# Performance work log

Measured on AMD Instinct MI355X. Metric: run time of the kernel, lower is better.

Reference implementation:

```python
import jax, jax.numpy as jnp
import numpy as np

EPS = 1e-5

@jax.custom_vjp
def binarize(x):
    return jnp.sign(x)

def _bin_fwd(x):
    return jnp.sign(x), None

def _bin_bwd(_, g):
    return (g,)  # straight-through estimator (matches .data overwrite trick)

binarize.defvjp(_bin_fwd, _bin_bwd)

def conv2d(x, w, b):
    y = jax.lax.conv_general_dilated(x, w, (1, 1), 'VALID',
                                     dimension_numbers=('NCHW', 'OIHW', 'NCHW'))
    return y + b[None, :, None, None]

def bn2d(x, g, be, m, v):
    inv = g / jnp.sqrt(v + EPS)
    return (x - m[None, :, None, None]) * inv[None, :, None, None] + be[None, :, None, None]

def bn1d(x, m, v):  # affine=False, eval mode
    return (x - m) / jnp.sqrt(v + EPS)

def maxpool2(x):
    return jax.lax.reduce_window(x, -jnp.inf, jax.lax.max, (1, 1, 2, 2), (1, 1, 2, 2), 'VALID')

def hardtanh(x):
    return jnp.clip(x, -1.0, 1.0)

def setup_inputs() -> dict:
    key = jax.random.key(0)
    ks = jax.random.split(key, 16)
    B = 8192
    d = {
        'x': jax.random.normal(ks[0], (B, 3, 32, 32), jnp.float32),
        'w1': jax.random.normal(ks[1], (16, 3, 5, 5), jnp.float32),
        'b1': jax.random.normal(ks[2], (16,), jnp.float32) * 0.1,
        'g1': jnp.ones((16,), jnp.float32), 'be1': jnp.zeros((16,), jnp.float32),
        'm1': jnp.zeros((16,), jnp.float32), 'v1': jnp.ones((16,), jnp.float32),
        'w2': jax.random.normal(ks[3], (32, 16, 5, 5), jnp.float32),
        'b2': jax.random.normal(ks[4], (32,), jnp.float32) * 0.1,
        'g2': jnp.ones((32,), jnp.float32), 'be2': jnp.zeros((32,), jnp.float32),
        'm2': jnp.zeros((32,), jnp.float32), 'v2': jnp.ones((32,), jnp.float32),
        'w3': jax.random.normal(ks[5], (64, 32, 5, 5), jnp.float32),
        'b3': jax.random.normal(ks[6], (64,), jnp.float32) * 0.1,
        'g3': jnp.ones((64,), jnp.float32), 'be3': jnp.zeros((64,), jnp.float32),
        'm3': jnp.zeros((64,), jnp.float32), 'v3': jnp.ones((64,), jnp.float32),
        'fw1': jax.random.normal(ks[7], (128, 64), jnp.float32),
        'fb1': jax.random.normal(ks[8], (128,), jnp.float32) * 0.1,
        'cm1': jnp.zeros((128,), jnp.float32), 'cv1': jnp.ones((128,), jnp.float32),
        'fw2': jax.random.normal(ks[9], (128, 128), jnp.float32),
        'fb2': jax.random.normal(ks[10], (128,), jnp.float32) * 0.1,
        'cm2': jnp.zeros((128,), jnp.float32), 'cv2': jnp.ones((128,), jnp.float32),
        'fw3': jax.random.normal(ks[11], (10, 128), jnp.float32),
        'cm3': jnp.zeros((10,), jnp.float32), 'cv3': jnp.ones((10,), jnp.float32),
    }
    return d

def reference(x, w1, b1, g1, be1, m1, v1, w2, b2, g2, be2, m2, v2,
              w3, b3, g3, be3, m3, v3, fw1, fb1, cm1, cv1,
              fw2, fb2, cm2, cv2, fw3, cm3, cv3):
    # features: conv1 input has 3 channels -> NOT binarized (first-layer rule)
    h = conv2d(x, binarize(w1), b1)
    h = maxpool2(hardtanh(bn2d(h, g1, be1, m1, v1)))
    h = conv2d(binarize(h), binarize(w2), b2)
    h = maxpool2(hardtanh(bn2d(h, g2, be2, m2, v2)))
    h = conv2d(binarize(h), binarize(w3), b3)
    h = hardtanh(bn2d(h, g3, be3, m3, v3))
    h = h.reshape(-1, 64)  # spatial is 1x1 by construction
    # classifier (all linear inputs binarized: in_features != 784)
    h = binarize(h) @ binarize(fw1).T + fb1
    h = bn1d(h, cm1, cv1)
    h = binarize(h) @ binarize(fw2).T + fb2
    h = bn1d(h, cm2, cv2)
    h = binarize(h) @ binarize(fw3).T
    h = bn1d(h, cm3, cv3)
    return jax.nn.log_softmax(h, axis=-1)
```

## Files before the change

### kernel.cpp

```cpp
#include <hip/hip_runtime.h>
#include <cstdint>

#define EPS 1e-5f

#define A1_OFF   0ull
#define W2M_OFF  4030464ull
#define W3M_OFF  4033664ull
#define FW1M_OFF 4040064ull
#define FW2M_OFF 4041088ull
#define FW3M_OFF 4043136ull
#define T1_OFF   4043296ull
#define T2_OFF   4043360ull
#define T3_OFF   4043488ull
#define TC1_OFF  4043744ull
#define TC2_OFF  4044256ull
#define BF_OFF   4044768ull
#define FIXCNT_OFF 4061184ull
#define FIXREC_OFF 4061248ull
#define FIXCAP   32768u

using bf16x8 = __attribute__((ext_vector_type(8))) short;
using f32x4  = __attribute__((ext_vector_type(4))) float;

union FragU { unsigned int u[4]; bf16x8 f; };

__device__ inline unsigned short rne_bf16(float f) {
    unsigned int u = __float_as_uint(f);
    return (unsigned short)((u + 0x7FFFu + ((u >> 16) & 1u)) >> 16);
}

__global__ void setup_kernel(
    const float* __restrict__ w1, const float* __restrict__ w2,
    const float* __restrict__ w3,
    const float* __restrict__ fw1, const float* __restrict__ fw2,
    const float* __restrict__ fw3,
    const float* __restrict__ b1, const float* __restrict__ g1,
    const float* __restrict__ be1, const float* __restrict__ m1,
    const float* __restrict__ v1,
    const float* __restrict__ b2, const float* __restrict__ g2,
    const float* __restrict__ be2, const float* __restrict__ m2,
    const float* __restrict__ v2,
    const float* __restrict__ b3, const float* __restrict__ g3,
    const float* __restrict__ be3, const float* __restrict__ m3,
    const float* __restrict__ v3,
    const float* __restrict__ fb1, const float* __restrict__ cm1,
    const float* __restrict__ fb2, const float* __restrict__ cm2,
    unsigned int* __restrict__ w2m, unsigned int* __restrict__ w3m,
    unsigned long long* __restrict__ fw1m, unsigned long long* __restrict__ fw2m,
    unsigned long long* __restrict__ fw3m,
    float* __restrict__ t1, float* __restrict__ t2, float* __restrict__ t3,
    float* __restrict__ tc1, float* __restrict__ tc2,
    uint4* __restrict__ bfrag, unsigned int* __restrict__ fixcnt)
{
    const int tid = threadIdx.x;
    const int blk = blockIdx.x;

    if (blk == 0) {
        if (tid < 16) t1[tid] = m1[tid] - be1[tid]*sqrtf(v1[tid]+EPS)/g1[tid] - b1[tid];
        if (tid < 32) t2[tid] = m2[tid] - be2[tid]*sqrtf(v2[tid]+EPS)/g2[tid] - b2[tid];
        if (tid < 64) t3[tid] = m3[tid] - be3[tid]*sqrtf(v3[tid]+EPS)/g3[tid] - b3[tid];
        if (tid < 128) { tc1[tid] = cm1[tid] - fb1[tid]; tc2[tid] = cm2[tid] - fb2[tid]; }
        for (int t = tid; t < 32*25; t += 256) {
            int oc = t / 25, pos = t % 25;
            unsigned int mk = 0;
            for (int ic = 0; ic < 16; ++ic)
                if (w2[(oc*16 + ic)*25 + pos] > 0.0f) mk |= 1u << ic;
            w2m[t] = mk;
        }
    } else if (blk == 1) {
        for (int t = tid; t < 64*25; t += 256) {
            int oc = t / 25, pos = t % 25;
            unsigned int mk = 0;
            for (int ic = 0; ic < 32; ++ic)
                if (w3[(oc*32 + ic)*25 + pos] > 0.0f) mk |= 1u << ic;
            w3m[t] = mk;
        }
    } else if (blk == 2) {
        for (int t = tid; t < 128; t += 256) {
            unsigned long long mk = 0;
            for (int i = 0; i < 64; ++i)
                if (fw1[t*64 + i] > 0.0f) mk |= 1ull << i;
            fw1m[t] = mk;
        }
    } else if (blk == 3) {
        for (int t = tid; t < 128; t += 256) {
            unsigned long long lo = 0, hi = 0;
            for (int i = 0; i < 64; ++i) {
                if (fw2[t*128 + i]      > 0.0f) lo |= 1ull << i;
                if (fw2[t*128 + 64 + i] > 0.0f) hi |= 1ull << i;
            }
            fw2m[2*t] = lo; fw2m[2*t+1] = hi;
        }
        if (tid < 10) {
            unsigned long long lo = 0, hi = 0;
            for (int i = 0; i < 64; ++i) {
                if (fw3[tid*128 + i]      > 0.0f) lo |= 1ull << i;
                if (fw3[tid*128 + 64 + i] > 0.0f) hi |= 1ull << i;
            }
            fw3m[2*tid] = lo; fw3m[2*tid+1] = hi;
        }
    } else {
        if (tid == 0) fixcnt[0] = 0;
        if (tid < 64) {
            const int oc = tid & 15, q = tid >> 4;
            for (int d = 0; d < 4; ++d)
                for (int kg = 0; kg < 4; ++kg) {
                    int ck = kg*4 + q;
                    unsigned short s[8];
                    for (int j = 0; j < 8; ++j) {
                        int kx = j - d;
                        unsigned short v = 0;
                        if (ck < 15 && kx >= 0 && kx < 5)
                            v = (w1[oc*75 + ck*5 + kx] > 0.0f) ? 0x3F80 : 0xBF80;
                        s[j] = v;
                    }
                    uint4 o;
                    o.x = (unsigned int)s[0] | ((unsigned int)s[1] << 16);
                    o.y = (unsigned int)s[2] | ((unsigned int)s[3] << 16);
                    o.z = (unsigned int)s[4] | ((unsigned int)s[5] << 16);
                    o.w = (unsigned int)s[6] | ((unsigned int)s[7] << 16);
                    bfrag[(d*4 + kg)*64 + tid] = o;
                }
        }
    }
}

__global__ __launch_bounds__(256, 3) void convpool1_kernel(
    const float* __restrict__ x, const float* __restrict__ t1,
    const uint4* __restrict__ bfrag, unsigned int* __restrict__ a1u,
    unsigned int* __restrict__ fixcnt, uint2* __restrict__ fixrec)
{
    __shared__ alignas(16) unsigned short xh[3*36*44];
    __shared__ alignas(16) unsigned short xl[3*36*44];
    __shared__ unsigned short pk16[196];

    const int tid  = threadIdx.x;
    const int lane = tid & 63;
    const int wv   = tid >> 6;
    const int quad = lane >> 4;
    const int me   = lane & 15;
    const int n0   = blockIdx.x * 8;

    FragU B[16];
    #pragma unroll
    for (int i = 0; i < 16; ++i)
        *(uint4*)B[i].u = bfrag[i*64 + lane];

    const float thr = t1[me];
    #pragma unroll 1
    for (int i = -1; i < 8; ++i) {
        float4 st[3];
        const int more = (i < 7);
        if (more) {
            const float4* xg = (const float4*)(x + (size_t)(n0 + i + 1) * 3072);
            #pragma unroll
            for (int k = 0; k < 3; ++k) st[k] = xg[tid + k*256];
        }

        if (i >= 0) {
            const int n = n0 + i;
            #pragma unroll 1
            for (int ti = 0; ti < 4; ++ti) {
                const int task = wv + ti*4;
                if (task >= 14) break;
                const int g = task >> 1, tt = task & 1;

                f32x4 acc[4];
                #pragma unroll
                for (int d = 0; d < 4; ++d) acc[d] = (f32x4){0.f, 0.f, 0.f, 0.f};

                #pragma unroll
                for (int kg = 0; kg < 4; ++kg) {
                    int ck = kg*4 + quad;
                    int ckc = ck < 15 ? ck : 14;
                    int c = ckc / 5, ky = ckc % 5;
                    int idx = (c*36 + ky + me + tt*16)*44 + 4*g;
                    FragU ah, al;
                    uint2 p0 = *(const uint2*)&xh[idx];
                    uint2 p1 = *(const uint2*)&xh[idx + 4];
                    ah.u[0] = p0.x; ah.u[1] = p0.y; ah.u[2] = p1.x; ah.u[3] = p1.y;
                    uint2 q0 = *(const uint2*)&xl[idx];
                    uint2 q1 = *(const uint2*)&xl[idx + 4];
                    al.u[0] = q0.x; al.u[1] = q0.y; al.u[2] = q1.x; al.u[3] = q1.y;
                    #pragma unroll
                    for (int d = 0; d < 4; ++d)
                        acc[d] = __builtin_amdgcn_mfma_f32_16x16x32_bf16(
                            ah.f, B[d*4 + kg].f, acc[d], 0, 0, 0);
                    #pragma unroll
                    for (int d = 0; d < 4; ++d)
                        acc[d] = __builtin_amdgcn_mfma_f32_16x16x32_bf16(
                            al.f, B[d*4 + kg].f, acc[d], 0, 0, 0);
                }

                const int valid = !(tt == 1 && quad == 3);
                #pragma unroll
                for (int dp = 0; dp < 2; ++dp) {
                    f32x4 A0 = acc[2*dp], A1 = acc[2*dp + 1];
                    #pragma unroll
                    for (int r = 0; r < 2; ++r) {
                        float h = fmaxf(fmaxf(A0[2*r], A0[2*r+1]),
                                        fmaxf(A1[2*r], A1[2*r+1]));
                        int bit = h > thr;
                        if (valid && fabsf(h - thr) < 2e-3f) {
                            int cell = (tt*8 + quad*2 + r)*14 + 2*g + dp;
                            unsigned int slot = atomicAdd(fixcnt, 1u);
                            if (slot < FIXCAP) {
                                uint2 rec;
                                rec.x = (unsigned int)n;
                                rec.y = ((unsigned int)cell << 8) | (unsigned int)me;
                                fixrec[slot] = rec;
                            }
                        }
                        unsigned long long mk = __ballot(bit);
                        if (me == 0 && valid)
                            pk16[(tt*8 + quad*2 + r)*14 + 2*g + dp] =
                                (unsigned short)(mk >> (quad*16));
                    }
                }
            }
        }
        __syncthreads();

        if (i >= 0 && tid < 98)
            a1u[(size_t)(n0 + i)*98 + tid] =
                (unsigned int)pk16[2*tid] | ((unsigned int)pk16[2*tid + 1] << 16);
        if (more) {
            #pragma unroll
            for (int k = 0; k < 3; ++k) {
                float4 v = st[k];
                int j = tid + k*256;
                int c = j >> 8, f = j & 255, row = f >> 3, q = f & 7;
                int e = (c*36 + row)*44 + 4*q;
                unsigned short h0 = rne_bf16(v.x), h1 = rne_bf16(v.y),
                               h2 = rne_bf16(v.z), h3 = rne_bf16(v.w);
                float r0 = v.x - __uint_as_float((unsigned int)h0 << 16);
                float r1 = v.y - __uint_as_float((unsigned int)h1 << 16);
                float r2 = v.z - __uint_as_float((unsigned int)h2 << 16);
                float r3 = v.w - __uint_as_float((unsigned int)h3 << 16);
                uint2 ph, pl;
                ph.x = (unsigned int)h0 | ((unsigned int)h1 << 16);
                ph.y = (unsigned int)h2 | ((unsigned int)h3 << 16);
                pl.x = (unsigned int)rne_bf16(r0) | ((unsigned int)rne_bf16(r1) << 16);
                pl.y = (unsigned int)rne_bf16(r2) | ((unsigned int)rne_bf16(r3) << 16);
                *(uint2*)&xh[e] = ph;
                *(uint2*)&xl[e] = pl;
            }
        }
        __syncthreads();
    }
}

__global__ void fixup_kernel(
    const float* __restrict__ x, const float* __restrict__ w1,
    const float* __restrict__ t1,
    const unsigned int* __restrict__ fixcnt, const uint2* __restrict__ fixrec,
    unsigned int* __restrict__ a1u)
{
    unsigned int cnt = fixcnt[0];
    if (cnt > FIXCAP) cnt = FIXCAP;
    for (unsigned int i = blockIdx.x*blockDim.x + threadIdx.x; i < cnt;
         i += gridDim.x*blockDim.x) {
        uint2 rec = fixrec[i];
        int n = (int)rec.x;
        int cell = (int)(rec.y >> 8);
        int oc = (int)(rec.y & 255u);
        int py = cell / 14, px = cell % 14;
        float thr = t1[oc];
        double best = -1e300;
        #pragma unroll 1
        for (int d2 = 0; d2 < 4; ++d2) {
            int oy = 2*py + (d2 >> 1), ox = 2*px + (d2 & 1);
            double s = 0.0;
            #pragma unroll 1
            for (int c2 = 0; c2 < 3; ++c2)
                #pragma unroll 1
                for (int ky2 = 0; ky2 < 5; ++ky2)
                    #pragma unroll 1
                    for (int kx2 = 0; kx2 < 5; ++kx2) {
                        float wv = w1[oc*75 + c2*25 + ky2*5 + kx2];
                        float xv = x[(size_t)n*3072 + c2*1024 + (oy + ky2)*32 + ox + kx2];
                        s += (wv > 0.0f) ? (double)xv : -(double)xv;
                    }
            best = fmax(best, s);
        }
        unsigned int mask = 1u << ((cell & 1)*16 + oc);
        unsigned int* wp = &a1u[(size_t)n*98 + (cell >> 1)];
        if (best > (double)thr) atomicOr(wp, mask);
        else                    atomicAnd(wp, ~mask);
    }
}

__global__ __launch_bounds__(256) void conv2tail_kernel(
    const unsigned int* __restrict__ a1u, const unsigned int* __restrict__ w2m,
    const float* __restrict__ t2,
    const unsigned int* __restrict__ w3m, const float* __restrict__ t3,
    const unsigned long long* __restrict__ fw1m, const float* __restrict__ tc1,
    const unsigned long long* __restrict__ fw2m, const float* __restrict__ tc2,
    const unsigned long long* __restrict__ fw3m,
    const float* __restrict__ cm3, const float* __restrict__ cv3,
    float* __restrict__ out)
{
    __shared__ unsigned int M[8][14][16];
    __shared__ unsigned int P[8][14][16];
    __shared__ unsigned int Q[8][13][16];
    __shared__ unsigned int a2l[8][25];
    __shared__ unsigned int w3s[1600];
    __shared__ unsigned long long fw1s[128], fw2s[256], fw3s[20];
    __shared__ float t3s[64], tc1s[128], tc2s[128], cm3s[16], cv3s[16];

    const int tid = threadIdx.x;
    const int lane = tid & 63;
    const int wv = tid >> 6;
    const int n0 = blockIdx.x * 8;

    for (int i = tid; i < 1600; i += 256) w3s[i] = w3m[i];
    if (tid < 128) { fw1s[tid] = fw1m[tid]; tc1s[tid] = tc1[tid]; tc2s[tid] = tc2[tid]; }
    fw2s[tid] = fw2m[tid];
    if (tid < 20) fw3s[tid] = fw3m[tid];
    if (tid < 64) t3s[tid] = t3[tid];
    if (tid < 10) { cm3s[tid] = cm3[tid]; cv3s[tid] = cv3[tid]; }

    for (int i = tid; i < 8*98; i += 256) {
        unsigned int v = a1u[(size_t)n0*98 + i];
        int e = 2*i;
        int im = e / 196, r = e - im*196;
        int y0 = r / 14, c0 = r - y0*14;
        int r1 = r + 1, y1 = r1 / 14, c1 = r1 - y1*14;
        M[im][y0][c0] = v & 0xffffu;
        M[im][y1][c1] = v >> 16;
    }
    __syncthreads();
    for (int i = tid; i < 8*14*13; i += 256) {
        int im = i / 182, r = i - im*182, y = r / 13, j = r - y*13;
        P[im][y][j] = M[im][y][j] | (M[im][y][j+1] << 16);
    }
    for (int i = tid; i < 8*13*14; i += 256) {
        int im = i / 182, r = i - im*182, y = r / 14, j = r - y*14;
        Q[im][y][j] = M[im][y][j] | (M[im][y+1][j] << 16);
    }
    __syncthreads();

    const int img = tid >> 5, oc = tid & 31;
    unsigned int wrow[25];
    #pragma unroll
    for (int k = 0; k < 25; ++k) wrow[k] = w2m[oc*25 + k];
    unsigned int wp[5][2], wc0, wc1, wcs;
    #pragma unroll
    for (int ky = 0; ky < 5; ++ky) {
        wp[ky][0] = wrow[ky*5]     | (wrow[ky*5+1] << 16);
        wp[ky][1] = wrow[ky*5 + 2] | (wrow[ky*5+3] << 16);
    }
    wc0 = wrow[4]  | (wrow[9]  << 16);
    wc1 = wrow[14] | (wrow[19] << 16);
    wcs = wrow[24];
    const float thr = t2[oc];

    unsigned int bits = 0;
    int hprev[5];
    #pragma unroll 2
    for (int oy = 0; oy < 10; ++oy) {
        unsigned int Pr[5][12];
        #pragma unroll
        for (int ky = 0; ky < 5; ++ky) {
            const uint4* pr = (const uint4*)&P[img][oy + ky][0];
            uint4 a = pr[0], b = pr[1], c = pr[2];
            Pr[ky][0]=a.x; Pr[ky][1]=a.y; Pr[ky][2]=a.z; Pr[ky][3]=a.w;
            Pr[ky][4]=b.x; Pr[ky][5]=b.y; Pr[ky][6]=b.z; Pr[ky][7]=b.w;
            Pr[ky][8]=c.x; Pr[ky][9]=c.y; Pr[ky][10]=c.z; Pr[ky][11]=c.w;
        }
        unsigned int Qa[10], Qb[10], Ms[10];
        {
            const uint4* qa = (const uint4*)&Q[img][oy][4];
            const uint2* qa2 = (const uint2*)&Q[img][oy][12];
            uint4 a = qa[0], b = qa[1]; uint2 c = qa2[0];
            Qa[0]=a.x; Qa[1]=a.y; Qa[2]=a.z; Qa[3]=a.w;
            Qa[4]=b.x; Qa[5]=b.y; Qa[6]=b.z; Qa[7]=b.w; Qa[8]=c.x; Qa[9]=c.y;
            const uint4* qb = (const uint4*)&Q[img][oy+2][4];
            const uint2* qb2 = (const uint2*)&Q[img][oy+2][12];
            uint4 d = qb[0], e = qb[1]; uint2 f = qb2[0];
            Qb[0]=d.x; Qb[1]=d.y; Qb[2]=d.z; Qb[3]=d.w;
            Qb[4]=e.x; Qb[5]=e.y; Qb[6]=e.z; Qb[7]=e.w; Qb[8]=f.x; Qb[9]=f.y;
            const uint4* ms = (const uint4*)&M[img][oy+4][4];
            const uint2* ms2 = (const uint2*)&M[img][oy+4][12];
            uint4 g = ms[0], h = ms[1]; uint2 k2 = ms2[0];
            Ms[0]=g.x; Ms[1]=g.y; Ms[2]=g.z; Ms[3]=g.w;
            Ms[4]=h.x; Ms[5]=h.y; Ms[6]=h.z; Ms[7]=h.w; Ms[8]=k2.x; Ms[9]=k2.y;
        }
        int X[10];
        #pragma unroll
        for (int ox = 0; ox < 10; ++ox) {
            int s = 0;
            #pragma unroll
            for (int ky = 0; ky < 5; ++ky)
                s += __popc(Pr[ky][ox] ^ wp[ky][0]) + __popc(Pr[ky][ox+2] ^ wp[ky][1]);
            s += __popc(Qa[ox] ^ wc0) + __popc(Qb[ox] ^ wc1) + __popc(Ms[ox] ^ wcs);
            X[ox] = s;
        }
        #pragma unroll
        for (int px = 0; px < 5; ++px) {
            int h = min(X[2*px], X[2*px+1]);
            if ((oy & 1) == 0) hprev[px] = h;
            else {
                int mn = min(hprev[px], h);
                if ((float)(400 - 2*mn) > thr) bits |= 1u << ((oy >> 1)*5 + px);
            }
        }
    }
    #pragma unroll
    for (int cell = 0; cell < 25; ++cell) {
        unsigned long long m = __ballot((bits >> cell) & 1);
        if (lane == 0)  a2l[2*wv][cell]     = (unsigned int)m;
        if (lane == 32) a2l[2*wv + 1][cell] = (unsigned int)(m >> 32);
    }
    __syncthreads();

    #pragma unroll 1
    for (int rnd = 0; rnd < 2; ++rnd) {
        const int im = wv + 4*rnd;
        const int n = n0 + im;

        unsigned int av[25];
        #pragma unroll
        for (int k = 0; k < 25; ++k) av[k] = a2l[im][k];

        int X = 0;
        #pragma unroll
        for (int k = 0; k < 25; ++k) X += __popc(av[k] ^ w3s[lane*25 + k]);
        float d3 = (float)(800 - 2*X);
        unsigned long long a3 = __ballot(d3 > t3s[lane]);

        int o1 = lane + 64;
        int d0 = 64 - 2*(int)__popcll(a3 ^ fw1s[lane]);
        int d1 = 64 - 2*(int)__popcll(a3 ^ fw1s[o1]);
        unsigned long long a4lo = __ballot((float)d0 > tc1s[lane]);
        unsigned long long a4hi = __ballot((float)d1 > tc1s[o1]);

        int e0 = 128 - 2*(int)(__popcll(a4lo ^ fw2s[2*lane]) + __popcll(a4hi ^ fw2s[2*lane+1]));
        int e1 = 128 - 2*(int)(__popcll(a4lo ^ fw2s[2*o1])   + __popcll(a4hi ^ fw2s[2*o1+1]));
        unsigned long long a5lo = __ballot((float)e0 > tc2s[lane]);
        unsigned long long a5hi = __ballot((float)e1 > tc2s[o1]);

        float y = -1e30f;
        if (lane < 10) {
            int f = 128 - 2*(int)(__popcll(a5lo ^ fw3s[2*lane]) + __popcll(a5hi ^ fw3s[2*lane+1]));
            y = ((float)f - cm3s[lane]) / sqrtf(cv3s[lane] + EPS);
        }
        float mx = y;
        #pragma unroll
        for (int off = 8; off > 0; off >>= 1) mx = fmaxf(mx, __shfl_xor(mx, off, 16));
        float s = (lane < 10) ? expf(y - mx) : 0.0f;
        #pragma unroll
        for (int off = 8; off > 0; off >>= 1) s += __shfl_xor(s, off, 16);
        if (lane < 10) out[(size_t)n*10 + lane] = y - mx - logf(s);
    }
}

extern "C" void kernel_launch(void* const* d_in, const int* in_sizes, int n_in,
                              void* d_out, int out_size, void* d_ws, size_t ws_size,
                              hipStream_t stream)
{
    const float* x   = (const float*)d_in[0];
    const float* w1  = (const float*)d_in[1];
    const float* b1  = (const float*)d_in[2];
    const float* g1  = (const float*)d_in[3];
    const float* be1 = (const float*)d_in[4];
    const float* m1  = (const float*)d_in[5];
    const float* v1  = (const float*)d_in[6];
    const float* w2  = (const float*)d_in[7];
    const float* b2  = (const float*)d_in[8];
    const float* g2  = (const float*)d_in[9];
    const float* be2 = (const float*)d_in[10];
    const float* m2  = (const float*)d_in[11];
    const float* v2  = (const float*)d_in[12];
    const float* w3  = (const float*)d_in[13];
    const float* b3  = (const float*)d_in[14];
    const float* g3  = (const float*)d_in[15];
    const float* be3 = (const float*)d_in[16];
    const float* m3  = (const float*)d_in[17];
    const float* v3  = (const float*)d_in[18];
    const float* fw1 = (const float*)d_in[19];
    const float* fb1 = (const float*)d_in[20];
    const float* cm1 = (const float*)d_in[21];
    const float* fw2 = (const float*)d_in[23];
    const float* fb2 = (const float*)d_in[24];
    const float* cm2 = (const float*)d_in[25];
    const float* fw3 = (const float*)d_in[27];
    const float* cm3 = (const float*)d_in[28];
    const float* cv3 = (const float*)d_in[29];

    char* ws = (char*)d_ws;
    unsigned int*       a1u  = (unsigned int*)(ws + A1_OFF);
    unsigned int*       w2m  = (unsigned int*)(ws + W2M_OFF);
    unsigned int*       w3m  = (unsigned int*)(ws + W3M_OFF);
    unsigned long long* fw1m = (unsigned long long*)(ws + FW1M_OFF);
    unsigned long long* fw2m = (unsigned long long*)(ws + FW2M_OFF);
    unsigned long long* fw3m = (unsigned long long*)(ws + FW3M_OFF);
    float* t1  = (float*)(ws + T1_OFF);
    float* t2  = (float*)(ws + T2_OFF);
    float* t3  = (float*)(ws + T3_OFF);
    float* tc1 = (float*)(ws + TC1_OFF);
    float* tc2 = (float*)(ws + TC2_OFF);
    uint4* bfrag = (uint4*)(ws + BF_OFF);
    unsigned int* fixcnt = (unsigned int*)(ws + FIXCNT_OFF);
    uint2* fixrec = (uint2*)(ws + FIXREC_OFF);

    setup_kernel<<<5, 256, 0, stream>>>(
        w1, w2, w3, fw1, fw2, fw3,
        b1, g1, be1, m1, v1,
        b2, g2, be2, m2, v2,
        b3, g3, be3, m3, v3,
        fb1, cm1, fb2, cm2,
        w2m, w3m, fw1m, fw2m, fw3m, t1, t2, t3, tc1, tc2, bfrag, fixcnt);

    convpool1_kernel<<<1024, 256, 0, stream>>>(x, t1, bfrag, a1u, fixcnt, fixrec);
    fixup_kernel<<<64, 256, 0, stream>>>(x, w1, t1, fixcnt, fixrec, a1u);
    conv2tail_kernel<<<1024, 256, 0, stream>>>(a1u, w2m, t2, w3m, t3,
                                               fw1m, tc1, fw2m, tc2, fw3m,
                                               cm3, cv3, (float*)d_out);
}
```

Before: 342.6 us.

## Shrink conv1 blocks to two waves, drop register prefetch, balance tasks per wave

The conv1+pool kernel now runs 128-thread blocks over 4 images each on a grid of 2048 blocks instead of 256 threads over 8 images. The register-staged prefetch of the next image is removed: each iteration loads and converts its own image, then syncs and computes. With two waves, each wave now handles exactly 7 of the 14 tasks, which removes the uneven 4/4/3/3 split. LDS base offsets are precomputed outside the loop. The aim is better wave balance, lower register pressure and more resident blocks, at the cost of losing the overlap between global loads and MFMA work inside a block.

```diff
diff --git a/kernel.cpp b/kernel.cpp
--- a/kernel.cpp
+++ b/kernel.cpp
@@ -125,7 +125,7 @@
     }
 }
 
-__global__ __launch_bounds__(256, 3) void convpool1_kernel(
+__global__ __launch_bounds__(128) void convpool1_kernel(
     const float* __restrict__ x, const float* __restrict__ t1,
     const uint4* __restrict__ bfrag, unsigned int* __restrict__ a1u,
     unsigned int* __restrict__ fixcnt, uint2* __restrict__ fixrec)
@@ -139,115 +139,121 @@
     const int wv   = tid >> 6;
     const int quad = lane >> 4;
     const int me   = lane & 15;
-    const int n0   = blockIdx.x * 8;
+    const int n0   = blockIdx.x * 4;
 
     FragU B[16];
     #pragma unroll
     for (int i = 0; i < 16; ++i)
         *(uint4*)B[i].u = bfrag[i*64 + lane];
 
+    int basekg[4];
+    #pragma unroll
+    for (int kg = 0; kg < 4; ++kg) {
+        int ck = kg*4 + quad;
+        int ckc = ck < 15 ? ck : 14;
+        int c = ckc / 5, ky = ckc % 5;
+        basekg[kg] = (c*36 + ky + me)*44;
+    }
+    int se[6];
+    #pragma unroll
+    for (int k = 0; k < 6; ++k) {
+        int j = tid + k*128;
+        int c = j >> 8, f = j & 255, row = f >> 3, q = f & 7;
+        se[k] = (c*36 + row)*44 + 4*q;
+    }
+
     const float thr = t1[me];
     #pragma unroll 1
-    for (int i = -1; i < 8; ++i) {
-        float4 st[3];
-        const int more = (i < 7);
-        if (more) {
-            const float4* xg = (const float4*)(x + (size_t)(n0 + i + 1) * 3072);
+    for (int i = 0; i < 4; ++i) {
+        if (i > 0 && tid < 98)
+            a1u[(size_t)(n0 + i - 1)*98 + tid] =
+                (unsigned int)pk16[2*tid] | ((unsigned int)pk16[2*tid + 1] << 16);
+        {
+            const float4* xg = (const float4*)(x + (size_t)(n0 + i) * 3072);
+            float4 v[6];
             #pragma unroll
-            for (int k = 0; k < 3; ++k) st[k] = xg[tid + k*256];
-        }
-
-        if (i >= 0) {
-            const int n = n0 + i;
-            #pragma unroll 1
-            for (int ti = 0; ti < 4; ++ti) {
-                const int task = wv + ti*4;
-                if (task >= 14) break;
-                const int g = task >> 1, tt = task & 1;
-
-                f32x4 acc[4];
-                #pragma unroll
-                for (int d = 0; d < 4; ++d) acc[d] = (f32x4){0.f, 0.f, 0.f, 0.f};
-
-                #pragma unroll
-                for (int kg = 0; kg < 4; ++kg) {
-                    int ck = kg*4 + quad;
-                    int ckc = ck < 15 ? ck : 14;
-                    int c = ckc / 5, ky = ckc % 5;
-                    int idx = (c*36 + ky + me + tt*16)*44 + 4*g;
-                    FragU ah, al;
-                    uint2 p0 = *(const uint2*)&xh[idx];
-                    uint2 p1 = *(const uint2*)&xh[idx + 4];
-                    ah.u[0] = p0.x; ah.u[1] = p0.y; ah.u[2] = p1.x; ah.u[3] = p1.y;
-                    uint2 q0 = *(const uint2*)&xl[idx];
-                    uint2 q1 = *(const uint2*)&xl[idx + 4];
-                    al.u[0] = q0.x; al.u[1] = q0.y; al.u[2] = q1.x; al.u[3] = q1.y;
-                    #pragma unroll
-                    for (int d = 0; d < 4; ++d)
-                        acc[d] = __builtin_amdgcn_mfma_f32_16x16x32_bf16(
-                            ah.f, B[d*4 + kg].f, acc[d], 0, 0, 0);
-                    #pragma unroll
-                    for (int d = 0; d < 4; ++d)
-                        acc[d] = __builtin_amdgcn_mfma_f32_16x16x32_bf16(
-                            al.f, B[d*4 + kg].f, acc[d], 0, 0, 0);
-                }
-
-                const int valid = !(tt == 1 && quad == 3);
-                #pragma unroll
-                for (int dp = 0; dp < 2; ++dp) {
-                    f32x4 A0 = acc[2*dp], A1 = acc[2*dp + 1];
-                    #pragma unroll
-                    for (int r = 0; r < 2; ++r) {
-                        float h = fmaxf(fmaxf(A0[2*r], A0[2*r+1]),
-                                        fmaxf(A1[2*r], A1[2*r+1]));
-                        int bit = h > thr;
-                        if (valid && fabsf(h - thr) < 2e-3f) {
-                            int cell = (tt*8 + quad*2 + r)*14 + 2*g + dp;
-                            unsigned int slot = atomicAdd(fixcnt, 1u);
-                            if (slot < FIXCAP) {
-                                uint2 rec;
-                                rec.x = (unsigned int)n;
-                                rec.y = ((unsigned int)cell << 8) | (unsigned int)me;
-                                fixrec[slot] = rec;
-                            }
-                        }
-                        unsigned long long mk = __ballot(bit);
-                        if (me == 0 && valid)
-                            pk16[(tt*8 + quad*2 + r)*14 + 2*g + dp] =
-                                (unsigned short)(mk >> (quad*16));
-                    }
-                }
-            }
-        }
-        __syncthreads();
-
-        if (i >= 0 && tid < 98)
-            a1u[(size_t)(n0 + i)*98 + tid] =
-                (unsigned int)pk16[2*tid] | ((unsigned int)pk16[2*tid + 1] << 16);
-        if (more) {
+            for (int k = 0; k < 6; ++k) v[k] = xg[tid + k*128];
             #pragma unroll
-            for (int k = 0; k < 3; ++k) {
-                float4 v = st[k];
-                int j = tid + k*256;
-                int c = j >> 8, f = j & 255, row = f >> 3, q = f & 7;
-                int e = (c*36 + row)*44 + 4*q;
-                unsigned short h0 = rne_bf16(v.x), h1 = rne_bf16(v.y),
-                               h2 = rne_bf16(v.z), h3 = rne_bf16(v.w);
-                float r0 = v.x - __uint_as_float((unsigned int)h0 << 16);
-                float r1 = v.y - __uint_as_float((unsigned int)h1 << 16);
-                float r2 = v.z - __uint_as_float((unsigned int)h2 << 16);
-                float r3 = v.w - __uint_as_float((unsigned int)h3 << 16);
+            for (int k = 0; k < 6; ++k) {
+                unsigned short h0 = rne_bf16(v[k].x), h1 = rne_bf16(v[k].y),
+                               h2 = rne_bf16(v[k].z), h3 = rne_bf16(v[k].w);
+                float r0 = v[k].x - __uint_as_float((unsigned int)h0 << 16);
+                float r1 = v[k].y - __uint_as_float((unsigned int)h1 << 16);
+                float r2 = v[k].z - __uint_as_float((unsigned int)h2 << 16);
+                float r3 = v[k].w - __uint_as_float((unsigned int)h3 << 16);
                 uint2 ph, pl;
                 ph.x = (unsigned int)h0 | ((unsigned int)h1 << 16);
                 ph.y = (unsigned int)h2 | ((unsigned int)h3 << 16);
                 pl.x = (unsigned int)rne_bf16(r0) | ((unsigned int)rne_bf16(r1) << 16);
                 pl.y = (unsigned int)rne_bf16(r2) | ((unsigned int)rne_bf16(r3) << 16);
-                *(uint2*)&xh[e] = ph;
-                *(uint2*)&xl[e] = pl;
+                *(uint2*)&xh[se[k]] = ph;
+                *(uint2*)&xl[se[k]] = pl;
             }
         }
         __syncthreads();
-    }
+
+        const int n = n0 + i;
+        #pragma unroll 1
+        for (int ti = 0; ti < 7; ++ti) {
+            const int task = wv*7 + ti;
+            const int g = task >> 1, tt = task & 1;
+            const int off = 4*g + tt*704;
+
+            f32x4 acc[4];
+            #pragma unroll
+            for (int d = 0; d < 4; ++d) acc[d] = (f32x4){0.f, 0.f, 0.f, 0.f};
+
+            #pragma unroll
+            for (int kg = 0; kg < 4; ++kg) {
+                int idx = basekg[kg] + off;
+                FragU ah, al;
+                uint2 p0 = *(const uint2*)&xh[idx];
+                uint2 p1 = *(const uint2*)&xh[idx + 4];
+                ah.u[0] = p0.x; ah.u[1] = p0.y; ah.u[2] = p1.x; ah.u[3] = p1.y;
+                uint2 q0 = *(const uint2*)&xl[idx];
+                uint2 q1 = *(const uint2*)&xl[idx + 4];
+                al.u[0] = q0.x; al.u[1] = q0.y; al.u[2] = q1.x; al.u[3] = q1.y;
+                #pragma unroll
+                for (int d = 0; d < 4; ++d)
+                    acc[d] = __builtin_amdgcn_mfma_f32_16x16x32_bf16(
+                        ah.f, B[d*4 + kg].f, acc[d], 0, 0, 0);
+                #pragma unroll
+                for (int d = 0; d < 4; ++d)
+                    acc[d] = __builtin_amdgcn_mfma_f32_16x16x32_bf16(
+                        al.f, B[d*4 + kg].f, acc[d], 0, 0, 0);
+            }
+
+            const int valid = !(tt == 1 && quad == 3);
+            #pragma unroll
+            for (int dp = 0; dp < 2; ++dp) {
+                f32x4 A0 = acc[2*dp], A1 = acc[2*dp + 1];
+                #pragma unroll
+                for (int r = 0; r < 2; ++r) {
+                    float h = fmaxf(fmaxf(A0[2*r], A0[2*r+1]),
+                                    fmaxf(A1[2*r], A1[2*r+1]));
+                    int bit = h > thr;
+                    if (valid && fabsf(h - thr) < 2e-3f) {
+                        int cell = (tt*8 + quad*2 + r)*14 + 2*g + dp;
+                        unsigned int slot = atomicAdd(fixcnt, 1u);
+                        if (slot < FIXCAP) {
+                            uint2 rec;
+                            rec.x = (unsigned int)n;
+                            rec.y = ((unsigned int)cell << 8) | (unsigned int)me;
+                            fixrec[slot] = rec;
+                        }
+                    }
+                    unsigned long long mk = __ballot(bit);
+                    if (me == 0 && valid)
+                        pk16[(tt*8 + quad*2 + r)*14 + 2*g + dp] =
+                            (unsigned short)(mk >> (quad*16));
+                }
+            }
+        }
+        __syncthreads();
+    }
+    if (tid < 98)
+        a1u[(size_t)(n0 + 3)*98 + tid] =
+            (unsigned int)pk16[2*tid] | ((unsigned int)pk16[2*tid + 1] << 16);
 }
 
 __global__ void fixup_kernel(
@@ -512,7 +518,7 @@
         fb1, cm1, fb2, cm2,
         w2m, w3m, fw1m, fw2m, fw3m, t1, t2, t3, tc1, tc2, bfrag, fixcnt);
 
-    convpool1_kernel<<<1024, 256, 0, stream>>>(x, t1, bfrag, a1u, fixcnt, fixrec);
+    convpool1_kernel<<<2048, 128, 0, stream>>>(x, t1, bfrag, a1u, fixcnt, fixrec);
     fixup_kernel<<<64, 256, 0, stream>>>(x, w1, t1, fixcnt, fixrec, a1u);
     conv2tail_kernel<<<1024, 256, 0, stream>>>(a1u, w2m, t2, w3m, t3,
                                                fw1m, tc1, fw2m, tc2, fw3m,
```

Result: faster. 329.3 us (-3.9%).
